# Optimization experiments

Hardware: AMD Instinct MI355X
Metric: run time of the kernel (lower is better)

The kernel has to match this reference:

```python
import jax, jax.numpy as jnp
import numpy as np
from jax import lax

NUM_CLASSES = 5
NUM_TASKS = 20
CONV_CHANS = [(64, 3), (64, 64), (128, 64), (128, 128), (256, 128), (256, 256)]  # (out, in)


def setup_inputs() -> dict:
    key = jax.random.key(0)
    ks = jax.random.split(key, 16)
    B = 512
    x = jax.random.normal(ks[0], (B, 3, 32, 32), dtype=jnp.float32)
    tid = jax.random.randint(ks[1], (B,), 0, NUM_TASKS)
    inp = {"x": x, "tid": tid}
    for i, (oc, ic) in enumerate(CONV_CHANS):
        fan_in = ic * 9
        inp[f"w{i}"] = jax.random.normal(ks[2 + 2 * i], (oc, ic, 3, 3), dtype=jnp.float32) * np.float32((2.0 / fan_in) ** 0.5)
        inp[f"b{i}"] = jnp.zeros((oc,), dtype=jnp.float32)
    inp["cw"] = jax.random.normal(ks[14], (NUM_CLASSES * NUM_TASKS, 4096), dtype=jnp.float32) * np.float32(4096 ** -0.5)
    inp["cb"] = jnp.zeros((NUM_CLASSES * NUM_TASKS,), dtype=jnp.float32)
    return inp


def _conv_relu(x, w, b):
    y = lax.conv_general_dilated(x, w, window_strides=(1, 1), padding='SAME',
                                 dimension_numbers=('NCHW', 'OIHW', 'NCHW'))
    return jax.nn.relu(y + b[None, :, None, None])


def _maxpool2(x):
    return lax.reduce_window(x, -jnp.inf, lax.max, (1, 1, 2, 2), (1, 1, 2, 2), 'VALID')


def _forward(x, tid, ws, bs, cw, cb):
    # VGG cfg [64,64,'M',128,128,'M',256,256,'M']
    h = _conv_relu(x, ws[0], bs[0])
    h = _conv_relu(h, ws[1], bs[1])
    h = _maxpool2(h)
    h = _conv_relu(h, ws[2], bs[2])
    h = _conv_relu(h, ws[3], bs[3])
    h = _maxpool2(h)
    h = _conv_relu(h, ws[4], bs[4])
    h = _conv_relu(h, ws[5], bs[5])
    h = _maxpool2(h)                      # [B, 256, 4, 4]
    feat = h.reshape(h.shape[0], -1)      # [B, 4096], matches torch NCHW flatten
    # Batched task-indexed classifier: gather each sample's 5-row weight block.
    w_sel = cw.reshape(NUM_TASKS, NUM_CLASSES, 4096)[tid]   # [B, 5, 4096]
    b_sel = cb.reshape(NUM_TASKS, NUM_CLASSES)[tid]         # [B, 5]
    return jnp.einsum('bcd,bd->bc', w_sel, feat) + b_sel


def reference(x, tid, w0, b0, w1, b1, w2, b2, w3, b3, w4, b4, w5, b5, cw, cb):
    ws = (w0, w1, w2, w3, w4, w5)
    bs = (b0, b1, b2, b3, b4, b5)
    return _forward(x, tid, ws, bs, cw, cb)
```

## Files before the change

kernel.cpp:

```cpp
#include <hip/hip_runtime.h>


typedef __attribute__((ext_vector_type(8))) short short8;
typedef __attribute__((ext_vector_type(4))) float floatx4;
typedef unsigned int uint;
typedef unsigned short ushort;

__device__ __forceinline__ ushort f2bf(float f) {
    uint u = __float_as_uint(f);
    return (ushort)((u + 0x7fffu + ((u >> 16) & 1u)) >> 16);
}
__device__ __forceinline__ float bf2f(ushort h) {
    return __uint_as_float(((uint)h) << 16);
}

typedef const __attribute__((address_space(1))) unsigned int* gas_ptr;
typedef __attribute__((address_space(3))) unsigned int* las_ptr;
__device__ __forceinline__ void gload_lds16(const void* g, void* l) {
    __builtin_amdgcn_global_load_lds((gas_ptr)g, (las_ptr)l, 16, 0, 0);
}

__device__ __forceinline__ void wlin_one(
    const float* __restrict__ src, short* __restrict__ dst, int OC, int IC, int o)
{
    int j    = o & 7;
    int lane = (o >> 3) & 63;
    int r    = o >> 9;
    int G16  = OC >> 4;
    int g    = r % G16;  r /= G16;
    int kk   = r % 9;
    int icb  = r / 9;
    int oc = g * 16 + (lane & 15);
    int ic = icb * 32 + (lane >> 4) * 8 + j;
    dst[o] = (short)f2bf(src[((long)oc * IC + ic) * 9 + kk]);
}

#define N_W0 2048
#define N_W1 36864
#define N_W2 73728
#define N_W3 147456
#define N_W4 294912
#define N_W5 589824
#define N_WT_TOTAL (N_W0 + N_W1 + N_W2 + N_W3 + N_W4 + N_W5)

__global__ __launch_bounds__(256) void wtransform_all(
    const float* __restrict__ w0, const float* __restrict__ w1,
    const float* __restrict__ w2, const float* __restrict__ w3,
    const float* __restrict__ w4, const float* __restrict__ w5,
    short* __restrict__ wt0, short* __restrict__ wts1, short* __restrict__ wts2,
    short* __restrict__ wts3, short* __restrict__ wts4, short* __restrict__ wts5,
    short* __restrict__ zp)
{
    if (blockIdx.x == 0 && threadIdx.x < 32) zp[threadIdx.x] = 0;
    int idx = blockIdx.x * 256 + threadIdx.x;
    if (idx < N_W0) {
        int oc = idx >> 5, k = idx & 31;
        wt0[idx] = (k < 27) ? (short)f2bf(w0[oc * 27 + k]) : (short)0;
        return;
    }
    idx -= N_W0;
    if (idx < N_W1) { wlin_one(w1, wts1, 64, 64, idx); return; }
    idx -= N_W1;
    if (idx < N_W2) { wlin_one(w2, wts2, 128, 64, idx); return; }
    idx -= N_W2;
    if (idx < N_W3) { wlin_one(w3, wts3, 128, 128, idx); return; }
    idx -= N_W3;
    if (idx < N_W4) { wlin_one(w4, wts4, 256, 128, idx); return; }
    idx -= N_W4;
    wlin_one(w5, wts5, 256, 256, idx);
}

__global__ __launch_bounds__(256, 2) void conv0_mfma(
    const float* __restrict__ x, const short* __restrict__ wT0,
    const float* __restrict__ b0, ushort* __restrict__ out)
{
    __shared__ float  s_x[3 * 18 * 34];
    __shared__ ushort s_b[4 * 512 * 8];

    const int tid  = threadIdx.x;
    const int wv   = tid >> 6;
    const int lane = tid & 63;
    const int quad = lane >> 4;
    const int l16  = lane & 15;
    const int b    = blockIdx.x >> 1;
    const int r0   = (blockIdx.x & 1) * 16;

    for (int idx = tid; idx < 3 * 18 * 34; idx += 256) {
        int c   = idx / 612;
        int rem = idx - c * 612;
        int ry  = rem / 34, rx = rem - ry * 34;
        int gy  = r0 + ry - 1, gx = rx - 1;
        float v = 0.f;
        if (gy >= 0 && gy < 32 && gx >= 0 && gx < 32)
            v = x[(((long)b * 3 + c) * 32 + gy) * 32 + gx];
        s_x[idx] = v;
    }
    __syncthreads();

#pragma unroll
    for (int rep = 0; rep < 2; ++rep) {
        int pxl = rep * 256 + tid;
        int py = pxl >> 5, px = pxl & 31;
        ushort v[32];
#pragma unroll
        for (int c = 0; c < 3; ++c)
#pragma unroll
            for (int ky = 0; ky < 3; ++ky)
#pragma unroll
                for (int kx = 0; kx < 3; ++kx)
                    v[c * 9 + ky * 3 + kx] = f2bf(s_x[c * 612 + (py + ky) * 34 + (px + kx)]);
#pragma unroll
        for (int k = 27; k < 32; ++k) v[k] = 0;
#pragma unroll
        for (int q = 0; q < 4; ++q)
            *(uint4*)(&s_b[(q * 512 + pxl) * 8]) = *(const uint4*)(v + q * 8);
    }
    __syncthreads();

    floatx4 acc[4][8];
#pragma unroll
    for (int i = 0; i < 4; ++i)
#pragma unroll
        for (int t = 0; t < 8; ++t) acc[i][t] = (floatx4)0.f;

    short8 afr[4];
#pragma unroll
    for (int i = 0; i < 4; ++i)
        afr[i] = *(const short8*)(wT0 + (i * 16 + l16) * 32 + quad * 8);
#pragma unroll
    for (int t = 0; t < 8; ++t) {
        int pxl = wv * 128 + t * 16 + l16;
        short8 bfr = *(const short8*)(&s_b[(quad * 512 + pxl) * 8]);
#pragma unroll
        for (int i = 0; i < 4; ++i)
            acc[i][t] = __builtin_amdgcn_mfma_f32_16x16x32_bf16(afr[i], bfr, acc[i][t], 0, 0, 0);
    }

#pragma unroll
    for (int i = 0; i < 4; ++i) {
        int oc0 = i * 16 + quad * 4;
        float4 bv = *(const float4*)(b0 + oc0);
#pragma unroll
        for (int t = 0; t < 8; ++t) {
            int pxl = wv * 128 + t * 16 + l16;
            int py = pxl >> 5, px = pxl & 31;
            long dst = ((((long)b * 8 + (oc0 >> 3)) * 32 + r0 + py) * 32 + px) * 8 + (oc0 & 7);
            float v0 = acc[i][t][0] + bv.x;
            float v1 = acc[i][t][1] + bv.y;
            float v2 = acc[i][t][2] + bv.z;
            float v3 = acc[i][t][3] + bv.w;
            ushort o[4];
            o[0] = f2bf(v0 > 0.f ? v0 : 0.f);
            o[1] = f2bf(v1 > 0.f ? v1 : 0.f);
            o[2] = f2bf(v2 > 0.f ? v2 : 0.f);
            o[3] = f2bf(v3 > 0.f ? v3 : 0.f);
            *(uint2*)(out + dst) = *(uint2*)o;
        }
    }
}

template<int IC, int OC, int H, int W, int ROWS, int OCGROUPS, bool POOL, bool CLS>
__global__ __launch_bounds__(256, 3) void conv_so(
    const ushort* __restrict__ act_in,
    const short*  __restrict__ wTs,
    const float*  __restrict__ bias,
    ushort* __restrict__ act_out,
    const ushort* __restrict__ zp,
    const int*   __restrict__ tids,
    const float* __restrict__ cw,
    const float* __restrict__ cbv,
    float*       __restrict__ outp)
{
    constexpr int WPAD  = W + 2;
    constexpr int RPAD  = ROWS + 2;
    constexpr int UNITS = RPAD * WPAD;
    constexpr int UNITSP = UNITS + 2;
    constexpr int SEGS  = H / ROWS;
    constexpr int C8I   = IC / 8;
    constexpr int G16   = OC / 16;
    constexpr int NICB  = IC / 32;
    constexpr int C8O   = OC / 8;
    constexpr int TMAX  = NICB * 9;
    constexpr int NSTG  = UNITSP * C8I;

    __shared__ ushort s_act[NSTG * 8];

    const int tid  = threadIdx.x;
    const int wv   = tid >> 6;
    const int lane = tid & 63;
    const int quad = lane >> 4;
    const int l16  = lane & 15;

    const int b   = blockIdx.x / SEGS;
    const int seg = blockIdx.x - b * SEGS;
    const int r0  = seg * ROWS;
    const int ocg = wv % OCGROUPS;
    const int pxg = wv / OCGROUPS;

    for (int c = tid; c < NSTG; c += 256) {
        int sub  = c / UNITSP;
        int unit = c - sub * UNITSP;
        int ry   = unit / WPAD, cx = unit - ry * WPAD;
        int gy   = r0 + ry - 1, gx = cx - 1;
        const ushort* src = zp;
        if (unit < UNITS && (unsigned)gy < (unsigned)H && (unsigned)gx < (unsigned)W)
            src = act_in + ((((long)b * C8I + sub) * H + gy) * W + gx) * 8;
        gload_lds16(src, &s_act[(size_t)(c - lane) * 8]);
    }
    __syncthreads();

    floatx4 acc[4][4];
#pragma unroll
    for (int i = 0; i < 4; ++i)
#pragma unroll
        for (int t = 0; t < 4; ++t) acc[i][t] = (floatx4)0.f;

    int bbase[4];
#pragma unroll
    for (int t = 0; t < 4; ++t) {
        int pxl = pxg * 64 + t * 16 + l16;
        int py  = pxl / W, px = pxl - py * W;
        bbase[t] = (py * WPAD + px) * 8;
    }

    const short8* wb = (const short8*)wTs;
    const int  wbase = (ocg * 4) * 64 + lane;
    const long WSTEP = (long)G16 * 64;

    short8 wpipe[3][4];
#pragma unroll
    for (int d = 0; d < 3; ++d)
#pragma unroll
        for (int i = 0; i < 4; ++i)
            wpipe[d][i] = wb[(long)d * WSTEP + wbase + i * 64];

    int tl = 0;
    for (int icb = 0; icb < NICB; ++icb) {
#pragma unroll
        for (int kk = 0; kk < 9; ++kk) {
            const int ky = kk / 3, kx = kk - ky * 3;
            const int koff = ((icb * 4 + quad) * UNITSP + ky * WPAD + kx) * 8;
            short8 bfr[4];
#pragma unroll
            for (int t = 0; t < 4; ++t)
                bfr[t] = *(const short8*)(&s_act[bbase[t] + koff]);
            const int slot = kk % 3;
#pragma unroll
            for (int i = 0; i < 4; ++i)
#pragma unroll
                for (int t = 0; t < 4; ++t)
                    acc[i][t] = __builtin_amdgcn_mfma_f32_16x16x32_bf16(
                        wpipe[slot][i], bfr[t], acc[i][t], 0, 0, 0);
            int tn = tl + 3;
            if (tn >= TMAX) tn = 0;
#pragma unroll
            for (int i = 0; i < 4; ++i)
                wpipe[slot][i] = wb[(long)tn * WSTEP + wbase + i * 64];
            ++tl;
        }
    }

    if constexpr (!POOL) {
#pragma unroll
        for (int i = 0; i < 4; ++i) {
            int oc0 = ocg * 64 + i * 16 + quad * 4;
            float4 bv = *(const float4*)(bias + oc0);
#pragma unroll
            for (int t = 0; t < 4; ++t) {
                int pxl = pxg * 64 + t * 16 + l16;
                int py  = pxl / W, px = pxl - py * W;
                long dst = ((((long)b * C8O + (oc0 >> 3)) * H + r0 + py) * W + px) * 8 + (oc0 & 7);
                float v0 = acc[i][t][0] + bv.x;
                float v1 = acc[i][t][1] + bv.y;
                float v2 = acc[i][t][2] + bv.z;
                float v3 = acc[i][t][3] + bv.w;
                ushort o[4];
                o[0] = f2bf(v0 > 0.f ? v0 : 0.f);
                o[1] = f2bf(v1 > 0.f ? v1 : 0.f);
                o[2] = f2bf(v2 > 0.f ? v2 : 0.f);
                o[3] = f2bf(v3 > 0.f ? v3 : 0.f);
                *(uint2*)(act_out + dst) = *(uint2*)o;
            }
        }
    } else {
        __syncthreads();
        ushort* s_pool = s_act;
        constexpr int PSTR = OC + 8;
        static_assert(ROWS * W * PSTR <= NSTG * 8, "pool scratch fits");
#pragma unroll
        for (int i = 0; i < 4; ++i) {
            int oc0 = ocg * 64 + i * 16 + quad * 4;
            float4 bv = *(const float4*)(bias + oc0);
#pragma unroll
            for (int t = 0; t < 4; ++t) {
                int pxl = pxg * 64 + t * 16 + l16;
                float v0 = acc[i][t][0] + bv.x;
                float v1 = acc[i][t][1] + bv.y;
                float v2 = acc[i][t][2] + bv.z;
                float v3 = acc[i][t][3] + bv.w;
                ushort o[4];
                o[0] = f2bf(v0 > 0.f ? v0 : 0.f);
                o[1] = f2bf(v1 > 0.f ? v1 : 0.f);
                o[2] = f2bf(v2 > 0.f ? v2 : 0.f);
                o[3] = f2bf(v3 > 0.f ? v3 : 0.f);
                *(uint2*)(&s_pool[pxl * PSTR + oc0]) = *(uint2*)o;
            }
        }
        __syncthreads();
        constexpr int PH = ROWS / 2, PW = W / 2, HOT = H / 2;
        const int pr0 = r0 / 2;
        ushort* s_feat = s_act + (NSTG * 8 - 4096);
        static_assert(!CLS || (ROWS * W * PSTR <= NSTG * 8 - 4096), "s_feat fits");
        static_assert(!CLS || (PH * PW == 16 && C8O * 8 == 256), "CLS geometry");
        for (int u = tid; u < PH * PW * C8O; u += 256) {
            int c8 = u % C8O;
            int pp = u / C8O;
            int xo = pp % PW, yo = pp / PW;
            const ushort* p00 = &s_pool[((2 * yo) * W + 2 * xo) * PSTR + c8 * 8];
            uint4 q0 = *(const uint4*)(p00);
            uint4 q1 = *(const uint4*)(p00 + PSTR);
            uint4 q2 = *(const uint4*)(p00 + W * PSTR);
            uint4 q3 = *(const uint4*)(p00 + W * PSTR + PSTR);
            const ushort* a0 = (const ushort*)&q0;
            const ushort* a1 = (const ushort*)&q1;
            const ushort* a2 = (const ushort*)&q2;
            const ushort* a3 = (const ushort*)&q3;
            ushort r[8];
#pragma unroll
            for (int j = 0; j < 8; ++j) {
                ushort m0 = a0[j] > a1[j] ? a0[j] : a1[j];
                ushort m1 = a2[j] > a3[j] ? a2[j] : a3[j];
                r[j] = m0 > m1 ? m0 : m1;
            }
            if constexpr (CLS) {
#pragma unroll
                for (int j = 0; j < 8; ++j)
                    s_feat[(c8 * 8 + j) * 16 + pp] = r[j];
            } else {
                long dst = ((((long)b * C8O + c8) * HOT + pr0 + yo) * PW + xo) * 8;
                *(uint4*)(act_out + dst) = *(uint4*)r;
            }
        }
        if constexpr (CLS) {
            __syncthreads();
            const int t = tids[b];
            const float* cbase = cw + (long)t * 5 * 4096;
            for (int c = wv; c < 5; c += 4) {
                const float* wrow = cbase + (long)c * 4096;
                float s = 0.f;
#pragma unroll 8
                for (int k = 0; k < 64; ++k)
                    s += wrow[lane + 64 * k] * bf2f(s_feat[lane + 64 * k]);
#pragma unroll
                for (int off = 32; off > 0; off >>= 1) s += __shfl_down(s, off, 64);
                if (lane == 0) outp[(long)b * 5 + c] = s + cbv[t * 5 + c];
            }
        }
    }
}

extern "C" void kernel_launch(void* const* d_in, const int* in_sizes, int n_in,
                              void* d_out, int out_size, void* d_ws, size_t ws_size,
                              hipStream_t stream)
{
    const float* x   = (const float*)d_in[0];
    const int*   tid = (const int*)d_in[1];
    const float* w0 = (const float*)d_in[2];  const float* b0 = (const float*)d_in[3];
    const float* w1 = (const float*)d_in[4];  const float* b1 = (const float*)d_in[5];
    const float* w2 = (const float*)d_in[6];  const float* b2 = (const float*)d_in[7];
    const float* w3 = (const float*)d_in[8];  const float* b3 = (const float*)d_in[9];
    const float* w4 = (const float*)d_in[10]; const float* b4 = (const float*)d_in[11];
    const float* w5 = (const float*)d_in[12]; const float* b5 = (const float*)d_in[13];
    const float* cw = (const float*)d_in[14];
    const float* cb = (const float*)d_in[15];
    float* outp = (float*)d_out;

    const int B = in_sizes[0] / (3 * 32 * 32);

    short* wt0  = (short*)d_ws;
    short* wts1 = wt0 + N_W0;
    short* wts2 = wts1 + N_W1;
    short* wts3 = wts2 + N_W2;
    short* wts4 = wts3 + N_W3;
    short* wts5 = wts4 + N_W4;
    short* zp   = wts5 + N_W5;
    const size_t WT_HW = (size_t)N_WT_TOTAL + 32;
    const size_t fixed_bytes = WT_HW * 2;

    int Bc = B;
    while (Bc > 2 && fixed_bytes + (size_t)Bc * 2 * 65536 * 2 > ws_size) Bc >>= 1;
    if (Bc < 2) Bc = 2;

    ushort* bufA = (ushort*)((short*)d_ws + WT_HW);
    ushort* bufB = bufA + (size_t)Bc * 65536;

    wtransform_all<<<(N_WT_TOTAL + 255) / 256, 256, 0, stream>>>(
        w0, w1, w2, w3, w4, w5, wt0, wts1, wts2, wts3, wts4, wts5, zp);

    for (int cb0 = 0; cb0 < B; cb0 += Bc) {
        const float* xc = x + (size_t)cb0 * 3 * 32 * 32;
        const int* tidc = tid + cb0;
        float* outc = outp + (size_t)cb0 * 5;

        conv0_mfma<<<Bc * 2, 256, 0, stream>>>(xc, wt0, b0, bufA);
        conv_so<64, 64, 32, 32, 8, 1, true, false><<<Bc * 4, 256, 0, stream>>>(
            bufA, wts1, b1, bufB, (ushort*)zp, nullptr, nullptr, nullptr, nullptr);
        conv_so<64, 128, 16, 16, 8, 2, false, false><<<Bc * 2, 256, 0, stream>>>(
            bufB, wts2, b2, bufA, (ushort*)zp, nullptr, nullptr, nullptr, nullptr);
        conv_so<128, 128, 16, 16, 8, 2, true, false><<<Bc * 2, 256, 0, stream>>>(
            bufA, wts3, b3, bufB, (ushort*)zp, nullptr, nullptr, nullptr, nullptr);
        conv_so<128, 256, 8, 8, 8, 4, false, false><<<Bc, 256, 0, stream>>>(
            bufB, wts4, b4, bufA, (ushort*)zp, nullptr, nullptr, nullptr, nullptr);
        conv_so<256, 256, 8, 8, 8, 4, true, true><<<Bc, 256, 0, stream>>>(
            bufA, wts5, b5, bufB, (ushort*)zp, tidc, cw, cb, outc);
    }
}
```

Baseline: 274.9 us.

## Double-buffer LDS activation fragments and use bf16 classifier weights

The conv main loop now processes pairs of input-channel blocks with 18 unrolled steps, prefetching the next step's B fragments from LDS into an alternate register set while the current MFMAs run. This is meant to hide LDS read latency behind MFMA work. The classifier weights are converted to bf16 in the weight-transform kernel and read as 16-byte vectors in the fused classifier. Launch bounds drop from 3 to 2 waves per SIMD to make room for the extra registers, which may lower occupancy. Rounding the classifier weights to bf16 also changes numerics slightly.

```diff
diff --git a/kernel.cpp b/kernel.cpp
--- a/kernel.cpp
+++ b/kernel.cpp
@@ -41,15 +41,18 @@
 #define N_W3 147456
 #define N_W4 294912
 #define N_W5 589824
+#define N_CWB (100 * 4096)
 #define N_WT_TOTAL (N_W0 + N_W1 + N_W2 + N_W3 + N_W4 + N_W5)
+#define N_ALL (N_WT_TOTAL + N_CWB)
 
 __global__ __launch_bounds__(256) void wtransform_all(
     const float* __restrict__ w0, const float* __restrict__ w1,
     const float* __restrict__ w2, const float* __restrict__ w3,
     const float* __restrict__ w4, const float* __restrict__ w5,
+    const float* __restrict__ cw,
     short* __restrict__ wt0, short* __restrict__ wts1, short* __restrict__ wts2,
     short* __restrict__ wts3, short* __restrict__ wts4, short* __restrict__ wts5,
-    short* __restrict__ zp)
+    short* __restrict__ zp, short* __restrict__ cwb)
 {
     if (blockIdx.x == 0 && threadIdx.x < 32) zp[threadIdx.x] = 0;
     int idx = blockIdx.x * 256 + threadIdx.x;
@@ -67,7 +70,9 @@
     idx -= N_W3;
     if (idx < N_W4) { wlin_one(w4, wts4, 256, 128, idx); return; }
     idx -= N_W4;
-    wlin_one(w5, wts5, 256, 256, idx);
+    if (idx < N_W5) { wlin_one(w5, wts5, 256, 256, idx); return; }
+    idx -= N_W5;
+    if (idx < N_CWB) cwb[idx] = (short)f2bf(cw[idx]);
 }
 
 __global__ __launch_bounds__(256, 2) void conv0_mfma(
@@ -160,14 +165,14 @@
 }
 
 template<int IC, int OC, int H, int W, int ROWS, int OCGROUPS, bool POOL, bool CLS>
-__global__ __launch_bounds__(256, 3) void conv_so(
+__global__ __launch_bounds__(256, 2) void conv_so(
     const ushort* __restrict__ act_in,
     const short*  __restrict__ wTs,
     const float*  __restrict__ bias,
     ushort* __restrict__ act_out,
     const ushort* __restrict__ zp,
     const int*   __restrict__ tids,
-    const float* __restrict__ cw,
+    const short* __restrict__ cwb,
     const float* __restrict__ cbv,
     float*       __restrict__ outp)
 {
@@ -182,6 +187,7 @@
     constexpr int C8O   = OC / 8;
     constexpr int TMAX  = NICB * 9;
     constexpr int NSTG  = UNITSP * C8I;
+    static_assert(NICB % 2 == 0, "icb pair unroll");
 
     __shared__ ushort s_act[NSTG * 8];
 
@@ -215,12 +221,12 @@
 #pragma unroll
         for (int t = 0; t < 4; ++t) acc[i][t] = (floatx4)0.f;
 
-    int bbase[4];
+    int bb[4];
 #pragma unroll
     for (int t = 0; t < 4; ++t) {
         int pxl = pxg * 64 + t * 16 + l16;
         int py  = pxl / W, px = pxl - py * W;
-        bbase[t] = (py * WPAD + px) * 8;
+        bb[t] = (py * WPAD + px) * 8 + quad * UNITSP * 8;
     }
 
     const short8* wb = (const short8*)wTs;
@@ -234,23 +240,44 @@
         for (int i = 0; i < 4; ++i)
             wpipe[d][i] = wb[(long)d * WSTEP + wbase + i * 64];
 
+    short8 bfrA[4], bfrB[4];
+#pragma unroll
+    for (int t = 0; t < 4; ++t)
+        bfrA[t] = *(const short8*)(&s_act[bb[t]]);
+
+    constexpr int ICB_STRIDE = 4 * UNITSP * 8;
     int tl = 0;
-    for (int icb = 0; icb < NICB; ++icb) {
-#pragma unroll
-        for (int kk = 0; kk < 9; ++kk) {
-            const int ky = kk / 3, kx = kk - ky * 3;
-            const int koff = ((icb * 4 + quad) * UNITSP + ky * WPAD + kx) * 8;
-            short8 bfr[4];
-#pragma unroll
-            for (int t = 0; t < 4; ++t)
-                bfr[t] = *(const short8*)(&s_act[bbase[t] + koff]);
-            const int slot = kk % 3;
-#pragma unroll
-            for (int i = 0; i < 4; ++i)
+    int kbase = 0;
+    for (int ic2 = 0; ic2 < NICB / 2; ++ic2) {
+        const int kwrap = (ic2 + 1 < NICB / 2) ? kbase + 2 * ICB_STRIDE : 0;
+#pragma unroll
+        for (int s = 0; s < 18; ++s) {
+            const int ns   = (s + 1) % 18;
+            const int nkk  = ns % 9;
+            const int ncst = (ns / 9) * ICB_STRIDE + ((nkk / 3) * WPAD + (nkk % 3)) * 8;
+            const int nbase = (s == 17) ? kwrap : kbase;
+            const int slot = s % 3;
+            if ((s & 1) == 0) {
 #pragma unroll
                 for (int t = 0; t < 4; ++t)
-                    acc[i][t] = __builtin_amdgcn_mfma_f32_16x16x32_bf16(
-                        wpipe[slot][i], bfr[t], acc[i][t], 0, 0, 0);
+                    bfrB[t] = *(const short8*)(&s_act[bb[t] + nbase + ncst]);
+#pragma unroll
+                for (int i = 0; i < 4; ++i)
+#pragma unroll
+                    for (int t = 0; t < 4; ++t)
+                        acc[i][t] = __builtin_amdgcn_mfma_f32_16x16x32_bf16(
+                            wpipe[slot][i], bfrA[t], acc[i][t], 0, 0, 0);
+            } else {
+#pragma unroll
+                for (int t = 0; t < 4; ++t)
+                    bfrA[t] = *(const short8*)(&s_act[bb[t] + nbase + ncst]);
+#pragma unroll
+                for (int i = 0; i < 4; ++i)
+#pragma unroll
+                    for (int t = 0; t < 4; ++t)
+                        acc[i][t] = __builtin_amdgcn_mfma_f32_16x16x32_bf16(
+                            wpipe[slot][i], bfrB[t], acc[i][t], 0, 0, 0);
+            }
             int tn = tl + 3;
             if (tn >= TMAX) tn = 0;
 #pragma unroll
@@ -258,6 +285,7 @@
                 wpipe[slot][i] = wb[(long)tn * WSTEP + wbase + i * 64];
             ++tl;
         }
+        kbase += 2 * ICB_STRIDE;
     }
 
     if constexpr (!POOL) {
@@ -344,13 +372,18 @@
         if constexpr (CLS) {
             __syncthreads();
             const int t = tids[b];
-            const float* cbase = cw + (long)t * 5 * 4096;
+            const short* cbase = cwb + (long)t * 5 * 4096;
             for (int c = wv; c < 5; c += 4) {
-                const float* wrow = cbase + (long)c * 4096;
+                const short* wrow = cbase + (long)c * 4096;
                 float s = 0.f;
-#pragma unroll 8
-                for (int k = 0; k < 64; ++k)
-                    s += wrow[lane + 64 * k] * bf2f(s_feat[lane + 64 * k]);
+#pragma unroll
+                for (int j = 0; j < 8; ++j) {
+                    short8 wv8 = *(const short8*)(wrow + lane * 8 + 512 * j);
+                    short8 fv8 = *(const short8*)(s_feat + lane * 8 + 512 * j);
+#pragma unroll
+                    for (int e = 0; e < 8; ++e)
+                        s += bf2f((ushort)wv8[e]) * bf2f((ushort)fv8[e]);
+                }
 #pragma unroll
                 for (int off = 32; off > 0; off >>= 1) s += __shfl_down(s, off, 64);
                 if (lane == 0) outp[(long)b * 5 + c] = s + cbv[t * 5 + c];
@@ -384,7 +417,8 @@
     short* wts4 = wts3 + N_W3;
     short* wts5 = wts4 + N_W4;
     short* zp   = wts5 + N_W5;
-    const size_t WT_HW = (size_t)N_WT_TOTAL + 32;
+    short* cwb  = zp + 32;
+    const size_t WT_HW = (size_t)N_WT_TOTAL + 32 + N_CWB;
     const size_t fixed_bytes = WT_HW * 2;
 
     int Bc = B;
@@ -394,8 +428,9 @@
     ushort* bufA = (ushort*)((short*)d_ws + WT_HW);
     ushort* bufB = bufA + (size_t)Bc * 65536;
 
-    wtransform_all<<<(N_WT_TOTAL + 255) / 256, 256, 0, stream>>>(
-        w0, w1, w2, w3, w4, w5, wt0, wts1, wts2, wts3, wts4, wts5, zp);
+    wtransform_all<<<(N_ALL + 255) / 256, 256, 0, stream>>>(
+        w0, w1, w2, w3, w4, w5, cw,
+        wt0, wts1, wts2, wts3, wts4, wts5, zp, cwb);
 
     for (int cb0 = 0; cb0 < B; cb0 += Bc) {
         const float* xc = x + (size_t)cb0 * 3 * 32 * 32;
@@ -412,6 +447,6 @@
         conv_so<128, 256, 8, 8, 8, 4, false, false><<<Bc, 256, 0, stream>>>(
             bufB, wts4, b4, bufA, (ushort*)zp, nullptr, nullptr, nullptr, nullptr);
         conv_so<256, 256, 8, 8, 8, 4, true, true><<<Bc, 256, 0, stream>>>(
-            bufA, wts5, b5, bufB, (ushort*)zp, tidc, cw, cb, outc);
-    }
-}
+            bufA, wts5, b5, bufB, (ushort*)zp, tidc, cwb, cb, outc);
+    }
+}
```

Result: slower. 322.2 us (+17.2%).
